# Optimization experiments

Measured on AMD Instinct MI355X. Metric: run time of the kernel, lower is better.

## Reference

```python
import jax, jax.numpy as jnp
import numpy as np

B, C, H, W = 8, 512, 96, 96
CQ = C // 8


def setup_inputs() -> dict:
    key = jax.random.key(0)
    ks = jax.random.split(key, 8)
    s = 1.0 / np.sqrt(C)  # conv-like init scale to keep logits sane
    return {
        "x": jax.random.normal(ks[0], (B, C, H, W), jnp.float32),
        "Wq": jax.random.normal(ks[1], (CQ, C), jnp.float32) * s,
        "bq": jax.random.normal(ks[2], (CQ,), jnp.float32) * s,
        "Wk": jax.random.normal(ks[3], (CQ, C), jnp.float32) * s,
        "bk": jax.random.normal(ks[4], (CQ,), jnp.float32) * s,
        "Wv": jax.random.normal(ks[5], (C, C), jnp.float32) * s,
        "bv": jax.random.normal(ks[6], (C,), jnp.float32) * s,
        "gamma": jax.random.normal(ks[7], (1,), jnp.float32),
    }


def reference(x, Wq, bq, Wk, bk, Wv, bv, gamma):
    # 1x1 convs == per-pixel linear projections
    q = jnp.einsum('bchw,oc->bohw', x, Wq) + bq[None, :, None, None]  # [B,CQ,H,W]
    k = jnp.einsum('bchw,oc->bohw', x, Wk) + bk[None, :, None, None]  # [B,CQ,H,W]
    v = jnp.einsum('bchw,oc->bohw', x, Wv) + bv[None, :, None, None]  # [B,C ,H,W]

    h = x.shape[2]
    # column (vertical) attention logits: query at (h,w) vs keys at (j,w)
    energy_H = jnp.einsum('bchw,bcjw->bhwj', q, k)  # [B,H,W,H]
    # row (horizontal) attention logits: query at (h,w) vs keys at (h,j)
    energy_W = jnp.einsum('bchw,bchj->bhwj', q, k)  # [B,H,W,W]

    att = jax.nn.softmax(jnp.concatenate([energy_H, energy_W], axis=-1), axis=-1)
    att_H = att[..., :h]   # [B,H,W,H]
    att_W = att[..., h:]   # [B,H,W,W]

    out_H = jnp.einsum('bcjw,bhwj->bchw', v, att_H)
    out_W = jnp.einsum('bchj,bhwj->bchw', v, att_W)
    return gamma[0] * (out_H + out_W)
```

## Files before the change

kernel.cpp:

```cpp
#include <hip/hip_runtime.h>

#define B 8
#define C 512
#define H 96
#define W 96
#define HW (H*W)
#define KD 512
#define NSP 9216

typedef __attribute__((ext_vector_type(4))) float f32x4;
typedef __attribute__((ext_vector_type(8))) _Float16 f16x8;

typedef __attribute__((address_space(3))) unsigned int lds_u32;
typedef const __attribute__((address_space(1))) unsigned int glb_u32;
static __device__ __forceinline__ void gload16(const void* gsrc, void* ldst) {
    __builtin_amdgcn_global_load_lds((glb_u32*)gsrc, (lds_u32*)ldst, 16, 0, 0);
}

static __device__ __forceinline__ int tidx(int row, int kgrp) {
    return row * 32 + ((kgrp ^ ((row >> 2) & 3)) << 3);
}
static __device__ __forceinline__ int tidx64(int row, int gr) {
    return row * 64 + ((gr ^ (row & 7)) << 3);
}

__global__ __launch_bounds__(256) void split_w(
    const float* __restrict__ Wv, const float* __restrict__ Wq, const float* __restrict__ Wk,
    _Float16* __restrict__ Wv_h,
    _Float16* __restrict__ Wqk_h, _Float16* __restrict__ Wqk_l)
{
    int i = blockIdx.x * 256 + threadIdx.x;
    if (i < C * C) Wv_h[i] = (_Float16)Wv[i];
    if (i < 128 * C) {
        int m = i / C, k = i % C;
        float f = (m < 64) ? Wq[m * C + k] : Wk[(m - 64) * C + k];
        _Float16 h = (_Float16)f;
        Wqk_h[i] = h;
        Wqk_l[i] = (_Float16)(f - (float)h);
    }
}

__global__ __launch_bounds__(256) void split_x(
    const float* __restrict__ x,
    _Float16* __restrict__ xhT, _Float16* __restrict__ xlT)
{
    __shared__ float t[64][65];
    int n0 = blockIdx.x * 64, k0 = blockIdx.y * 64, b = blockIdx.z;
    int tid = threadIdx.x;
    const float* xb = x + ((size_t)b * KD + k0) * NSP + n0;
    #pragma unroll
    for (int it = 0; it < 4; ++it) {
        int idx = tid + it * 256;
        int kr = idx >> 4, nq = idx & 15;
        float4 v = *(const float4*)&xb[(size_t)kr * NSP + nq * 4];
        t[kr][nq * 4 + 0] = v.x;
        t[kr][nq * 4 + 1] = v.y;
        t[kr][nq * 4 + 2] = v.z;
        t[kr][nq * 4 + 3] = v.w;
    }
    __syncthreads();
    #pragma unroll
    for (int it = 0; it < 2; ++it) {
        int gid = tid + it * 256;
        int n = gid >> 3, g = gid & 7;
        f16x8 hi, lo;
        #pragma unroll
        for (int u = 0; u < 8; ++u) {
            float f = t[g * 8 + u][n];
            _Float16 hh = (_Float16)f;
            hi[u] = hh;
            lo[u] = (_Float16)(f - (float)hh);
        }
        size_t off = ((size_t)b * NSP + n0 + n) * KD + k0 + g * 8;
        *(f16x8*)&xhT[off] = hi;
        *(f16x8*)&xlT[off] = lo;
    }
}

__global__ __launch_bounds__(256, 2) void gemm_v(
    const _Float16* __restrict__ xhT,
    const _Float16* __restrict__ Wh,
    const float* __restrict__ bias,
    _Float16* __restrict__ out16)
{
    __shared__ _Float16 smem[8192];
    const int W_OFF = 0, X_OFF = 4096;

    int tid = threadIdx.x;
    int n0 = blockIdx.x * 128, m0 = blockIdx.y * 128, b = blockIdx.z;
    int lane = tid & 63, wave = tid >> 6;
    int wr = wave >> 1, wc = wave & 1;
    int l15 = lane & 15, l4 = lane >> 4;

    int grow = tid >> 2, gcol = (tid & 3) * 8;
    const _Float16* pW = Wh + (size_t)(m0 + grow) * KD + gcol;
    const _Float16* pX = xhT + ((size_t)b * NSP + n0 + grow) * KD + gcol;
    const size_t half = (size_t)64 * KD;
    int ldsW0 = W_OFF + wave * 512;
    int ldsW1 = W_OFF + 2048 + wave * 512;
    int ldsX0 = X_OFF + wave * 512;
    int ldsX1 = X_OFF + 2048 + wave * 512;

    f32x4 acc[4][4];
    #pragma unroll
    for (int i = 0; i < 4; ++i)
        #pragma unroll
        for (int j = 0; j < 4; ++j)
            acc[i][j] = (f32x4){0.f, 0.f, 0.f, 0.f};

    for (int k0 = 0; k0 < KD; k0 += 32) {
        gload16(pW + k0,        &smem[ldsW0]);
        gload16(pW + half + k0, &smem[ldsW1]);
        gload16(pX + k0,        &smem[ldsX0]);
        gload16(pX + half + k0, &smem[ldsX1]);
        __syncthreads();

        f16x8 af[4], bf[4];
        #pragma unroll
        for (int f = 0; f < 4; ++f) {
            af[f] = *(const f16x8*)&smem[W_OFF + (wr * 64 + f * 16 + l15) * 32 + l4 * 8];
            bf[f] = *(const f16x8*)&smem[X_OFF + (wc * 64 + f * 16 + l15) * 32 + l4 * 8];
        }
        #pragma unroll
        for (int i = 0; i < 4; ++i)
            #pragma unroll
            for (int j = 0; j < 4; ++j)
                acc[i][j] = __builtin_amdgcn_mfma_f32_16x16x32_f16(af[i], bf[j], acc[i][j], 0, 0, 0);
        __syncthreads();
    }

    #pragma unroll
    for (int i = 0; i < 4; ++i)
        #pragma unroll
        for (int r = 0; r < 4; ++r) {
            int row = m0 + wr * 64 + i * 16 + l4 * 4 + r;
            float bv = bias[row];
            #pragma unroll
            for (int j = 0; j < 4; ++j) {
                int col = n0 + wc * 64 + j * 16 + l15;
                out16[((size_t)b * C + row) * NSP + col] = (_Float16)(acc[i][j][r] + bv);
            }
        }
}

__global__ __launch_bounds__(256, 2) void gemm_qk(
    const _Float16* __restrict__ xhT, const _Float16* __restrict__ xlT,
    const _Float16* __restrict__ Wqh, const _Float16* __restrict__ Wql,
    const float* __restrict__ bias0, const float* __restrict__ bias1,
    _Float16* __restrict__ qh, _Float16* __restrict__ ql,
    _Float16* __restrict__ kh, _Float16* __restrict__ kl)
{
    __shared__ _Float16 smem[16384];
    const int XH = 0, XL = 4096, WHo = 8192, WLo = 12288;

    int tid = threadIdx.x;
    int n0 = blockIdx.x * 128, b = blockIdx.z;
    int lane = tid & 63, wave = tid >> 6;
    int wr = wave >> 1, wc = wave & 1;
    int l15 = lane & 15, l4 = lane >> 4;

    int grow = tid >> 2, gcol = (tid & 3) * 8;
    const _Float16* pXh = xhT + ((size_t)b * NSP + n0 + grow) * KD + gcol;
    const _Float16* pXl = xlT + ((size_t)b * NSP + n0 + grow) * KD + gcol;
    const _Float16* pWh = Wqh + (size_t)grow * KD + gcol;
    const _Float16* pWl = Wql + (size_t)grow * KD + gcol;
    const size_t half = (size_t)64 * KD;
    int base0 = wave * 512, base1 = 2048 + wave * 512;

    f32x4 acc[4][4];
    #pragma unroll
    for (int i = 0; i < 4; ++i)
        #pragma unroll
        for (int j = 0; j < 4; ++j)
            acc[i][j] = (f32x4){0.f, 0.f, 0.f, 0.f};

    for (int k0 = 0; k0 < KD; k0 += 32) {
        gload16(pXh + k0,        &smem[XH + base0]);
        gload16(pXh + half + k0, &smem[XH + base1]);
        gload16(pXl + k0,        &smem[XL + base0]);
        gload16(pXl + half + k0, &smem[XL + base1]);
        gload16(pWh + k0,        &smem[WHo + base0]);
        gload16(pWh + half + k0, &smem[WHo + base1]);
        gload16(pWl + k0,        &smem[WLo + base0]);
        gload16(pWl + half + k0, &smem[WLo + base1]);
        __syncthreads();

        f16x8 axh[4], axl[4], bwh[4], bwl[4];
        #pragma unroll
        for (int f = 0; f < 4; ++f) {
            int ra = (wr * 64 + f * 16 + l15) * 32 + l4 * 8;
            int rb = (wc * 64 + f * 16 + l15) * 32 + l4 * 8;
            axh[f] = *(const f16x8*)&smem[XH + ra];
            axl[f] = *(const f16x8*)&smem[XL + ra];
            bwh[f] = *(const f16x8*)&smem[WHo + rb];
            bwl[f] = *(const f16x8*)&smem[WLo + rb];
        }
        #pragma unroll
        for (int i = 0; i < 4; ++i)
            #pragma unroll
            for (int j = 0; j < 4; ++j)
                acc[i][j] = __builtin_amdgcn_mfma_f32_16x16x32_f16(axh[i], bwh[j], acc[i][j], 0, 0, 0);
        #pragma unroll
        for (int i = 0; i < 4; ++i)
            #pragma unroll
            for (int j = 0; j < 4; ++j)
                acc[i][j] = __builtin_amdgcn_mfma_f32_16x16x32_f16(axh[i], bwl[j], acc[i][j], 0, 0, 0);
        #pragma unroll
        for (int i = 0; i < 4; ++i)
            #pragma unroll
            for (int j = 0; j < 4; ++j)
                acc[i][j] = __builtin_amdgcn_mfma_f32_16x16x32_f16(axl[i], bwh[j], acc[i][j], 0, 0, 0);
        __syncthreads();
    }

    #pragma unroll
    for (int i = 0; i < 4; ++i)
        #pragma unroll
        for (int r = 0; r < 4; ++r) {
            int sp = n0 + wr * 64 + i * 16 + l4 * 4 + r;
            #pragma unroll
            for (int j = 0; j < 4; ++j) {
                int wcol = wc * 64 + j * 16 + l15;
                float val = acc[i][j][r] + (wcol < 64 ? bias0[wcol] : bias1[wcol - 64]);
                _Float16 hi = (_Float16)val;
                _Float16 lo = (_Float16)(val - (float)hi);
                size_t off = ((size_t)b * NSP + sp) * 64 + (wcol & 63);
                if (wcol < 64) { qh[off] = hi; ql[off] = lo; }
                else           { kh[off] = hi; kl[off] = lo; }
            }
        }
}

__global__ __launch_bounds__(256, 2) void energy_mfma(
    const _Float16* __restrict__ qh, const _Float16* __restrict__ ql,
    const _Float16* __restrict__ kh, const _Float16* __restrict__ kl,
    float* __restrict__ out, float* __restrict__ part, int pMul, int rMul)
{
    __shared__ _Float16 sm[4 * 96 * 64];
    const int T_QH = 0, T_QL = 6144, T_KH = 12288, T_KL = 18432;
    int p = blockIdx.x, b = blockIdx.y;
    int tid = threadIdx.x;
    size_t base = ((size_t)b * HW + (size_t)p * pMul) * 64;
    size_t rstride = (size_t)rMul * 64;

    #pragma unroll
    for (int tile = 0; tile < 4; ++tile) {
        const _Float16* src = (tile == 0) ? qh : (tile == 1) ? ql : (tile == 2) ? kh : kl;
        int tb = tile * 6144;
        #pragma unroll
        for (int sub = 0; sub < 3; ++sub) {
            int s = sub * 256 + tid;
            int row = s >> 3, g = s & 7;
            f16x8 d = *(const f16x8*)&src[base + row * rstride + g * 8];
            *(f16x8*)&sm[tb + tidx64(row, g)] = d;
        }
    }
    __syncthreads();

    int lane = tid & 63, wave = tid >> 6;
    int wr = wave >> 1, wc = wave & 1;
    int l15 = lane & 15, l4 = lane >> 4;

    f32x4 acc[3][3];
    #pragma unroll
    for (int i = 0; i < 3; ++i)
        #pragma unroll
        for (int j = 0; j < 3; ++j)
            acc[i][j] = (f32x4){0.f, 0.f, 0.f, 0.f};

    #pragma unroll
    for (int ks = 0; ks < 2; ++ks) {
        f16x8 Ah[3], Al[3], Bh[3], Bl[3];
        int gr = ks * 4 + l4;
        #pragma unroll
        for (int i = 0; i < 3; ++i) {
            int sa = tidx64(wr * 48 + i * 16 + l15, gr);
            Ah[i] = *(const f16x8*)&sm[T_QH + sa];
            Al[i] = *(const f16x8*)&sm[T_QL + sa];
            int sb = tidx64(wc * 48 + i * 16 + l15, gr);
            Bh[i] = *(const f16x8*)&sm[T_KH + sb];
            Bl[i] = *(const f16x8*)&sm[T_KL + sb];
        }
        #pragma unroll
        for (int i = 0; i < 3; ++i)
            #pragma unroll
            for (int j = 0; j < 3; ++j) {
                acc[i][j] = __builtin_amdgcn_mfma_f32_16x16x32_f16(Ah[i], Bh[j], acc[i][j], 0, 0, 0);
                acc[i][j] = __builtin_amdgcn_mfma_f32_16x16x32_f16(Ah[i], Bl[j], acc[i][j], 0, 0, 0);
                acc[i][j] = __builtin_amdgcn_mfma_f32_16x16x32_f16(Al[i], Bh[j], acc[i][j], 0, 0, 0);
            }
    }

    size_t ob = (size_t)(b * 96 + p) * 9216;
    #pragma unroll
    for (int i = 0; i < 3; ++i)
        #pragma unroll
        for (int r = 0; r < 4; ++r) {
            int row = wr * 48 + i * 16 + l4 * 4 + r;
            #pragma unroll
            for (int j = 0; j < 3; ++j)
                out[ob + (size_t)row * 96 + wc * 48 + j * 16 + l15] = acc[i][j][r];
        }

    __syncthreads();
    float* scr = (float*)sm;
    #pragma unroll
    for (int i = 0; i < 3; ++i)
        #pragma unroll
        for (int r = 0; r < 4; ++r) {
            int row = wr * 48 + i * 16 + l4 * 4 + r;
            float m3 = fmaxf(fmaxf(acc[i][0][r], acc[i][1][r]), acc[i][2][r]);
            #pragma unroll
            for (int mk = 1; mk < 16; mk <<= 1) m3 = fmaxf(m3, __shfl_xor(m3, mk));
            float s = __expf(acc[i][0][r] - m3) + __expf(acc[i][1][r] - m3) + __expf(acc[i][2][r] - m3);
            #pragma unroll
            for (int mk = 1; mk < 16; mk <<= 1) s += __shfl_xor(s, mk);
            if (l15 == 0) {
                scr[row * 4 + wc * 2]     = m3;
                scr[row * 4 + wc * 2 + 1] = s;
            }
        }
    __syncthreads();
    if (tid < 96) {
        float m0 = scr[tid * 4], s0 = scr[tid * 4 + 1];
        float m1 = scr[tid * 4 + 2], s1 = scr[tid * 4 + 3];
        float M = fmaxf(m0, m1);
        float S = s0 * __expf(m0 - M) + s1 * __expf(m1 - M);
        size_t idx = (pMul == 96) ? ((size_t)b * HW + p * 96 + tid)
                                  : ((size_t)b * HW + tid * 96 + p);
        part[idx * 2]     = M;
        part[idx * 2 + 1] = S;
    }
}

__global__ __launch_bounds__(256) void combine_ms(
    const float* __restrict__ pW, const float* __restrict__ pH,
    const float* __restrict__ gamma, float* __restrict__ ms)
{
    int row = blockIdx.x * 256 + threadIdx.x;
    float mW = pW[row * 2], sW = pW[row * 2 + 1];
    float mH = pH[row * 2], sH = pH[row * 2 + 1];
    float M = fmaxf(mW, mH);
    float S = sW * __expf(mW - M) + sH * __expf(mH - M);
    ms[row * 2]     = M;
    ms[row * 2 + 1] = gamma[0] / S;
}

template<int OUT16>
__global__ __launch_bounds__(256) void agg_mfma(
    const float* __restrict__ E, const float* __restrict__ ms,
    const _Float16* __restrict__ v16,
    float* __restrict__ dstF, _Float16* __restrict__ dstH, int msMode)
{
    __shared__ _Float16 satt[3][96 * 32];

    int r = blockIdx.x, b = blockIdx.y;
    int tid = threadIdx.x;
    int lane = tid & 63, wave = tid >> 6;
    int l15 = lane & 15, l4 = lane >> 4;

    const float* Eb = &E[(size_t)(b * 96 + r) * 9216];
    int msBase = b * HW;
    #pragma unroll
    for (int it = 0; it < 5; ++it) {
        int g_id = tid + it * 256;
        if (g_id < 1152) {
            int s = g_id / 12, gj = g_id % 12;
            int mi = msMode ? (msBase + s * 96 + r) : (msBase + r * 96 + s);
            float m  = ms[(size_t)mi * 2];
            float sc = ms[(size_t)mi * 2 + 1];
            float4 e0 = *(const float4*)&Eb[s * 96 + gj * 8];
            float4 e1 = *(const float4*)&Eb[s * 96 + gj * 8 + 4];
            float pv[8] = {e0.x, e0.y, e0.z, e0.w, e1.x, e1.y, e1.z, e1.w};
            f16x8 ph;
            #pragma unroll
            for (int u = 0; u < 8; ++u)
                ph[u] = (_Float16)(__expf(pv[u] - m) * sc);
            *(f16x8*)&satt[gj >> 2][tidx(s, gj & 3)] = ph;
        }
    }
    __syncthreads();

    const _Float16* vb = v16 + (size_t)b * C * 9216 + r * 96;

    for (int cc = 0; cc < 4; ++cc) {
        int cbase = cc * 128 + wave * 32;
        f32x4 acc[2][6];
        #pragma unroll
        for (int i = 0; i < 2; ++i)
            #pragma unroll
            for (int n = 0; n < 6; ++n)
                acc[i][n] = (f32x4){0.f, 0.f, 0.f, 0.f};

        #pragma unroll
        for (int kc = 0; kc < 3; ++kc) {
            f16x8 af[2];
            #pragma unroll
            for (int i = 0; i < 2; ++i)
                af[i] = *(const f16x8*)&vb[(size_t)(cbase + i * 16 + l15) * 9216 + kc * 32 + l4 * 8];
            f16x8 Bp[6];
            #pragma unroll
            for (int n = 0; n < 6; ++n)
                Bp[n] = *(const f16x8*)&satt[kc][tidx(n * 16 + l15, l4)];
            #pragma unroll
            for (int i = 0; i < 2; ++i)
                #pragma unroll
                for (int n = 0; n < 6; ++n)
                    acc[i][n] = __builtin_amdgcn_mfma_f32_16x16x32_f16(af[i], Bp[n], acc[i][n], 0, 0, 0);
        }

        #pragma unroll
        for (int i = 0; i < 2; ++i)
            #pragma unroll
            for (int r4 = 0; r4 < 4; ++r4) {
                int cl = cbase + i * 16 + l4 * 4 + r4;
                size_t rowb = ((size_t)b * C + cl) * 9216 + r * 96;
                #pragma unroll
                for (int n = 0; n < 6; ++n) {
                    int s = n * 16 + l15;
                    if (OUT16) dstH[rowb + s] = (_Float16)acc[i][n][r4];
                    else       dstF[rowb + s] = acc[i][n][r4];
                }
            }
    }
}

__global__ __launch_bounds__(256) void transpose_f16(
    const _Float16* __restrict__ src, _Float16* __restrict__ dst)
{
    size_t base = (size_t)blockIdx.x * (96 * 96);
    __shared__ _Float16 t[96][97];
    int tid = threadIdx.x;
    for (int i = tid; i < 96 * 96; i += 256) t[i / 96][i % 96] = src[base + i];
    __syncthreads();
    for (int i = tid; i < 96 * 96; i += 256) dst[base + i] = t[i % 96][i / 96];
}

__global__ __launch_bounds__(256) void transpose_add(
    const _Float16* __restrict__ srcT, float* __restrict__ out)
{
    size_t base = (size_t)blockIdx.x * (96 * 96);
    __shared__ _Float16 t[96][97];
    int tid = threadIdx.x;
    for (int i = tid; i < 96 * 96; i += 256) t[i / 96][i % 96] = srcT[base + i];
    __syncthreads();
    for (int i = tid; i < 96 * 96; i += 256) out[base + i] += (float)t[i % 96][i / 96];
}

__global__ __launch_bounds__(256) void combine(
    const _Float16* __restrict__ w16, const _Float16* __restrict__ hT,
    float* __restrict__ out)
{
    size_t base = (size_t)blockIdx.x * (96 * 96);
    __shared__ _Float16 t[96][97];
    int tid = threadIdx.x;
    for (int i = tid; i < 96 * 96; i += 256) t[i / 96][i % 96] = hT[base + i];
    __syncthreads();
    for (int i = tid; i < 96 * 96; i += 256)
        out[base + i] = (float)w16[base + i] + (float)t[i % 96][i / 96];
}

extern "C" void kernel_launch(void* const* d_in, const int* in_sizes, int n_in,
                              void* d_out, int out_size, void* d_ws, size_t ws_size,
                              hipStream_t stream)
{
    const float* x     = (const float*)d_in[0];
    const float* Wq    = (const float*)d_in[1];
    const float* bq    = (const float*)d_in[2];
    const float* Wk    = (const float*)d_in[3];
    const float* bk    = (const float*)d_in[4];
    const float* Wv    = (const float*)d_in[5];
    const float* bv    = (const float*)d_in[6];
    const float* gamma = (const float*)d_in[7];
    float* out = (float*)d_out;

    const size_t NK = (size_t)B * NSP * KD;
    _Float16* xhT = (_Float16*)d_ws;
    _Float16* xlT = xhT + NK;
    _Float16* qh  = xlT + NK;
    _Float16* ql  = qh + (size_t)B * HW * 64;
    _Float16* kh  = ql + (size_t)B * HW * 64;
    _Float16* kl  = kh + (size_t)B * HW * 64;
    float* EHp = (float*)(kl + (size_t)B * HW * 64);
    float* EWp = EHp + (size_t)B * HW * 96;
    float* ms  = (float*)qh;
    _Float16* vA  = xlT;
    _Float16* vB  = xhT;
    _Float16* outHT = xlT;
    float* pW = (float*)xhT;
    float* pH = pW + (size_t)2 * B * HW;

    _Float16* Wv_h  = (_Float16*)EHp;
    _Float16* Wqk_h = Wv_h + (size_t)C * C;
    _Float16* Wqk_l = Wqk_h + (size_t)128 * C;

    const size_t NEED = 245366784ull;
    bool bigws = ws_size >= NEED + NK * sizeof(_Float16);
    _Float16* outW16 = (_Float16*)((char*)d_ws + NEED);

    dim3 blk(256);

    split_w<<<dim3((C*C + 255)/256), blk, 0, stream>>>(Wv, Wq, Wk, Wv_h, Wqk_h, Wqk_l);
    split_x<<<dim3(NSP/64, KD/64, B), blk, 0, stream>>>(x, xhT, xlT);

    gemm_qk<<<dim3(NSP/128, 1, B), blk, 0, stream>>>(xhT, xlT, Wqk_h, Wqk_l, bq, bk, qh, ql, kh, kl);
    gemm_v<<<dim3(NSP/128, C/128, B), blk, 0, stream>>>(xhT, Wv_h, bv, vA);

    energy_mfma<<<dim3(96, B), blk, 0, stream>>>(qh, ql, kh, kl, EWp, pW, 96, 1);
    energy_mfma<<<dim3(96, B), blk, 0, stream>>>(qh, ql, kh, kl, EHp, pH, 1, 96);
    combine_ms<<<dim3(B*HW/256), blk, 0, stream>>>(pW, pH, gamma, ms);

    transpose_f16<<<dim3(B*C), blk, 0, stream>>>(vA, vB);

    if (bigws) {
        agg_mfma<1><<<dim3(96, B), blk, 0, stream>>>(EWp, ms, vA, nullptr, outW16, 0);
        agg_mfma<1><<<dim3(96, B), blk, 0, stream>>>(EHp, ms, vB, nullptr, outHT, 1);
        combine<<<dim3(B*C), blk, 0, stream>>>(outW16, outHT, out);
    } else {
        agg_mfma<0><<<dim3(96, B), blk, 0, stream>>>(EWp, ms, vA, out, nullptr, 0);
        agg_mfma<1><<<dim3(96, B), blk, 0, stream>>>(EHp, ms, vB, nullptr, outHT, 1);
        transpose_add<<<dim3(B*C), blk, 0, stream>>>(outHT, out);
    }
}
```

Before: 378.2 us.

## Store energy logits as max-subtracted fp16, vectorize transposes, add nontemporal memory ops

Energy kernels now subtract the per-row partial max and write the logits as fp16 instead of fp32. This halves the energy write and read traffic, and each agg kernel can exponentiate directly using a per-direction scale precomputed in combine_ms. split_x processes two k-tiles per block with batched loads, and the transpose and combine kernels use 16-byte vector loads and stores. Nontemporal hints are added across many stores. fp16 logits lose some precision, and the row-max exponent trick assumes (logit - partial max) plus a scale stays in range.

```diff
diff --git a/kernel.cpp b/kernel.cpp
--- a/kernel.cpp
+++ b/kernel.cpp
@@ -44,36 +44,43 @@
     const float* __restrict__ x,
     _Float16* __restrict__ xhT, _Float16* __restrict__ xlT)
 {
-    __shared__ float t[64][65];
-    int n0 = blockIdx.x * 64, k0 = blockIdx.y * 64, b = blockIdx.z;
+    __shared__ float t[2][64][65];
+    int n0 = blockIdx.x * 64, k0 = blockIdx.y * 128, b = blockIdx.z;
     int tid = threadIdx.x;
     const float* xb = x + ((size_t)b * KD + k0) * NSP + n0;
+
+    f32x4 v[8];
+    #pragma unroll
+    for (int it = 0; it < 8; ++it) {
+        int idx = tid + it * 256;
+        int tile = idx >> 10, kr = (idx >> 4) & 63, nq = idx & 15;
+        v[it] = __builtin_nontemporal_load(
+            (const f32x4*)&xb[(size_t)(tile * 64 + kr) * NSP + nq * 4]);
+    }
+    #pragma unroll
+    for (int it = 0; it < 8; ++it) {
+        int idx = tid + it * 256;
+        int tile = idx >> 10, kr = (idx >> 4) & 63, nq = idx & 15;
+        #pragma unroll
+        for (int u = 0; u < 4; ++u) t[tile][kr][nq * 4 + u] = v[it][u];
+    }
+    __syncthreads();
     #pragma unroll
     for (int it = 0; it < 4; ++it) {
-        int idx = tid + it * 256;
-        int kr = idx >> 4, nq = idx & 15;
-        float4 v = *(const float4*)&xb[(size_t)kr * NSP + nq * 4];
-        t[kr][nq * 4 + 0] = v.x;
-        t[kr][nq * 4 + 1] = v.y;
-        t[kr][nq * 4 + 2] = v.z;
-        t[kr][nq * 4 + 3] = v.w;
-    }
-    __syncthreads();
-    #pragma unroll
-    for (int it = 0; it < 2; ++it) {
         int gid = tid + it * 256;
-        int n = gid >> 3, g = gid & 7;
+        int tile = gid >> 9, w2 = gid & 511;
+        int n = w2 >> 3, g = w2 & 7;
         f16x8 hi, lo;
         #pragma unroll
         for (int u = 0; u < 8; ++u) {
-            float f = t[g * 8 + u][n];
+            float f = t[tile][g * 8 + u][n];
             _Float16 hh = (_Float16)f;
             hi[u] = hh;
             lo[u] = (_Float16)(f - (float)hh);
         }
-        size_t off = ((size_t)b * NSP + n0 + n) * KD + k0 + g * 8;
-        *(f16x8*)&xhT[off] = hi;
-        *(f16x8*)&xlT[off] = lo;
+        size_t off = ((size_t)b * NSP + n0 + n) * KD + k0 + tile * 64 + g * 8;
+        __builtin_nontemporal_store(hi, (f16x8*)&xhT[off]);
+        __builtin_nontemporal_store(lo, (f16x8*)&xlT[off]);
     }
 }
 
@@ -138,7 +145,8 @@
             #pragma unroll
             for (int j = 0; j < 4; ++j) {
                 int col = n0 + wc * 64 + j * 16 + l15;
-                out16[((size_t)b * C + row) * NSP + col] = (_Float16)(acc[i][j][r] + bv);
+                __builtin_nontemporal_store((_Float16)(acc[i][j][r] + bv),
+                    &out16[((size_t)b * C + row) * NSP + col]);
             }
         }
 }
@@ -234,7 +242,7 @@
 __global__ __launch_bounds__(256, 2) void energy_mfma(
     const _Float16* __restrict__ qh, const _Float16* __restrict__ ql,
     const _Float16* __restrict__ kh, const _Float16* __restrict__ kl,
-    float* __restrict__ out, float* __restrict__ part, int pMul, int rMul)
+    _Float16* __restrict__ out16, float* __restrict__ part, int pMul, int rMul)
 {
     __shared__ _Float16 sm[4 * 96 * 64];
     const int T_QH = 0, T_QL = 6144, T_KH = 12288, T_KL = 18432;
@@ -291,19 +299,9 @@
             }
     }
 
-    size_t ob = (size_t)(b * 96 + p) * 9216;
-    #pragma unroll
-    for (int i = 0; i < 3; ++i)
-        #pragma unroll
-        for (int r = 0; r < 4; ++r) {
-            int row = wr * 48 + i * 16 + l4 * 4 + r;
-            #pragma unroll
-            for (int j = 0; j < 3; ++j)
-                out[ob + (size_t)row * 96 + wc * 48 + j * 16 + l15] = acc[i][j][r];
-        }
-
-    __syncthreads();
-    float* scr = (float*)sm;
+    __syncthreads();
+    float* scr  = (float*)sm;
+    float* scrM = scr + 384;
     #pragma unroll
     for (int i = 0; i < 3; ++i)
         #pragma unroll
@@ -330,25 +328,42 @@
                                   : ((size_t)b * HW + tid * 96 + p);
         part[idx * 2]     = M;
         part[idx * 2 + 1] = S;
-    }
+        scrM[tid] = M;
+    }
+    __syncthreads();
+
+    size_t ob = (size_t)(b * 96 + p) * 9216;
+    #pragma unroll
+    for (int i = 0; i < 3; ++i)
+        #pragma unroll
+        for (int r = 0; r < 4; ++r) {
+            int row = wr * 48 + i * 16 + l4 * 4 + r;
+            float Mrow = scrM[row];
+            #pragma unroll
+            for (int j = 0; j < 3; ++j)
+                __builtin_nontemporal_store((_Float16)(acc[i][j][r] - Mrow),
+                    &out16[ob + (size_t)row * 96 + wc * 48 + j * 16 + l15]);
+        }
 }
 
 __global__ __launch_bounds__(256) void combine_ms(
     const float* __restrict__ pW, const float* __restrict__ pH,
-    const float* __restrict__ gamma, float* __restrict__ ms)
+    const float* __restrict__ gamma,
+    float* __restrict__ msW, float* __restrict__ msH)
 {
     int row = blockIdx.x * 256 + threadIdx.x;
     float mW = pW[row * 2], sW = pW[row * 2 + 1];
     float mH = pH[row * 2], sH = pH[row * 2 + 1];
     float M = fmaxf(mW, mH);
-    float S = sW * __expf(mW - M) + sH * __expf(mH - M);
-    ms[row * 2]     = M;
-    ms[row * 2 + 1] = gamma[0] / S;
+    float eW = __expf(mW - M), eH = __expf(mH - M);
+    float g = gamma[0] / (sW * eW + sH * eH);
+    msW[row] = g * eW;
+    msH[row] = g * eH;
 }
 
 template<int OUT16>
 __global__ __launch_bounds__(256) void agg_mfma(
-    const float* __restrict__ E, const float* __restrict__ ms,
+    const _Float16* __restrict__ E16, const float* __restrict__ msDir,
     const _Float16* __restrict__ v16,
     float* __restrict__ dstF, _Float16* __restrict__ dstH, int msMode)
 {
@@ -359,7 +374,7 @@
     int lane = tid & 63, wave = tid >> 6;
     int l15 = lane & 15, l4 = lane >> 4;
 
-    const float* Eb = &E[(size_t)(b * 96 + r) * 9216];
+    const _Float16* Eb = &E16[(size_t)(b * 96 + r) * 9216];
     int msBase = b * HW;
     #pragma unroll
     for (int it = 0; it < 5; ++it) {
@@ -367,15 +382,12 @@
         if (g_id < 1152) {
             int s = g_id / 12, gj = g_id % 12;
             int mi = msMode ? (msBase + s * 96 + r) : (msBase + r * 96 + s);
-            float m  = ms[(size_t)mi * 2];
-            float sc = ms[(size_t)mi * 2 + 1];
-            float4 e0 = *(const float4*)&Eb[s * 96 + gj * 8];
-            float4 e1 = *(const float4*)&Eb[s * 96 + gj * 8 + 4];
-            float pv[8] = {e0.x, e0.y, e0.z, e0.w, e1.x, e1.y, e1.z, e1.w};
+            float sc = msDir[mi];
+            f16x8 ev = *(const f16x8*)&Eb[s * 96 + gj * 8];
             f16x8 ph;
             #pragma unroll
             for (int u = 0; u < 8; ++u)
-                ph[u] = (_Float16)(__expf(pv[u] - m) * sc);
+                ph[u] = (_Float16)(__expf((float)ev[u]) * sc);
             *(f16x8*)&satt[gj >> 2][tidx(s, gj & 3)] = ph;
         }
     }
@@ -418,8 +430,8 @@
                 #pragma unroll
                 for (int n = 0; n < 6; ++n) {
                     int s = n * 16 + l15;
-                    if (OUT16) dstH[rowb + s] = (_Float16)acc[i][n][r4];
-                    else       dstF[rowb + s] = acc[i][n][r4];
+                    if (OUT16) __builtin_nontemporal_store((_Float16)acc[i][n][r4], &dstH[rowb + s]);
+                    else       __builtin_nontemporal_store(acc[i][n][r4], &dstF[rowb + s]);
                 }
             }
     }
@@ -429,20 +441,34 @@
     const _Float16* __restrict__ src, _Float16* __restrict__ dst)
 {
     size_t base = (size_t)blockIdx.x * (96 * 96);
-    __shared__ _Float16 t[96][97];
-    int tid = threadIdx.x;
-    for (int i = tid; i < 96 * 96; i += 256) t[i / 96][i % 96] = src[base + i];
-    __syncthreads();
-    for (int i = tid; i < 96 * 96; i += 256) dst[base + i] = t[i % 96][i / 96];
+    __shared__ _Float16 t[96][104];
+    int tid = threadIdx.x;
+    for (int g = tid; g < 1152; g += 256) {
+        int row = g / 12, c8 = (g % 12) * 8;
+        f16x8 v = __builtin_nontemporal_load((const f16x8*)&src[base + row * 96 + c8]);
+        *(f16x8*)&t[row][c8] = v;
+    }
+    __syncthreads();
+    for (int g = tid; g < 1152; g += 256) {
+        int row = g / 12, c8 = (g % 12) * 8;
+        f16x8 o;
+        #pragma unroll
+        for (int u = 0; u < 8; ++u) o[u] = t[c8 + u][row];
+        __builtin_nontemporal_store(o, (f16x8*)&dst[base + row * 96 + c8]);
+    }
 }
 
 __global__ __launch_bounds__(256) void transpose_add(
     const _Float16* __restrict__ srcT, float* __restrict__ out)
 {
     size_t base = (size_t)blockIdx.x * (96 * 96);
-    __shared__ _Float16 t[96][97];
-    int tid = threadIdx.x;
-    for (int i = tid; i < 96 * 96; i += 256) t[i / 96][i % 96] = srcT[base + i];
+    __shared__ _Float16 t[96][104];
+    int tid = threadIdx.x;
+    for (int g = tid; g < 1152; g += 256) {
+        int row = g / 12, c8 = (g % 12) * 8;
+        f16x8 v = *(const f16x8*)&srcT[base + row * 96 + c8];
+        *(f16x8*)&t[row][c8] = v;
+    }
     __syncthreads();
     for (int i = tid; i < 96 * 96; i += 256) out[base + i] += (float)t[i % 96][i / 96];
 }
@@ -452,12 +478,25 @@
     float* __restrict__ out)
 {
     size_t base = (size_t)blockIdx.x * (96 * 96);
-    __shared__ _Float16 t[96][97];
-    int tid = threadIdx.x;
-    for (int i = tid; i < 96 * 96; i += 256) t[i / 96][i % 96] = hT[base + i];
-    __syncthreads();
-    for (int i = tid; i < 96 * 96; i += 256)
-        out[base + i] = (float)w16[base + i] + (float)t[i % 96][i / 96];
+    __shared__ _Float16 t[96][104];
+    int tid = threadIdx.x;
+    for (int g = tid; g < 1152; g += 256) {
+        int row = g / 12, c8 = (g % 12) * 8;
+        f16x8 v = __builtin_nontemporal_load((const f16x8*)&hT[base + row * 96 + c8]);
+        *(f16x8*)&t[row][c8] = v;
+    }
+    __syncthreads();
+    for (int g = tid; g < 1152; g += 256) {
+        int row = g / 12, c8 = (g % 12) * 8;
+        f16x8 wv = __builtin_nontemporal_load((const f16x8*)&w16[base + row * 96 + c8]);
+        f32x4 o0, o1;
+        #pragma unroll
+        for (int u = 0; u < 4; ++u) o0[u] = (float)wv[u] + (float)t[c8 + u][row];
+        #pragma unroll
+        for (int u = 0; u < 4; ++u) o1[u] = (float)wv[4 + u] + (float)t[c8 + 4 + u][row];
+        __builtin_nontemporal_store(o0, (f32x4*)&out[base + row * 96 + c8]);
+        __builtin_nontemporal_store(o1, (f32x4*)&out[base + row * 96 + c8 + 4]);
+    }
 }
 
 extern "C" void kernel_launch(void* const* d_in, const int* in_sizes, int n_in,
@@ -481,16 +520,19 @@
     _Float16* ql  = qh + (size_t)B * HW * 64;
     _Float16* kh  = ql + (size_t)B * HW * 64;
     _Float16* kl  = kh + (size_t)B * HW * 64;
-    float* EHp = (float*)(kl + (size_t)B * HW * 64);
-    float* EWp = EHp + (size_t)B * HW * 96;
-    float* ms  = (float*)qh;
+    float* R4f = (float*)(kl + (size_t)B * HW * 64);
+    float* R5f = R4f + (size_t)B * HW * 96;
+    _Float16* EH16 = (_Float16*)R4f;
+    _Float16* EW16 = (_Float16*)R5f;
+    float* msW = (float*)qh;
+    float* msH = msW + (size_t)B * HW;
     _Float16* vA  = xlT;
     _Float16* vB  = xhT;
     _Float16* outHT = xlT;
     float* pW = (float*)xhT;
     float* pH = pW + (size_t)2 * B * HW;
 
-    _Float16* Wv_h  = (_Float16*)EHp;
+    _Float16* Wv_h  = (_Float16*)R4f;
     _Float16* Wqk_h = Wv_h + (size_t)C * C;
     _Float16* Wqk_l = Wqk_h + (size_t)128 * C;
 
@@ -501,24 +543,24 @@
     dim3 blk(256);
 
     split_w<<<dim3((C*C + 255)/256), blk, 0, stream>>>(Wv, Wq, Wk, Wv_h, Wqk_h, Wqk_l);
-    split_x<<<dim3(NSP/64, KD/64, B), blk, 0, stream>>>(x, xhT, xlT);
+    split_x<<<dim3(NSP/64, KD/128, B), blk, 0, stream>>>(x, xhT, xlT);
 
     gemm_qk<<<dim3(NSP/128, 1, B), blk, 0, stream>>>(xhT, xlT, Wqk_h, Wqk_l, bq, bk, qh, ql, kh, kl);
     gemm_v<<<dim3(NSP/128, C/128, B), blk, 0, stream>>>(xhT, Wv_h, bv, vA);
 
-    energy_mfma<<<dim3(96, B), blk, 0, stream>>>(qh, ql, kh, kl, EWp, pW, 96, 1);
-    energy_mfma<<<dim3(96, B), blk, 0, stream>>>(qh, ql, kh, kl, EHp, pH, 1, 96);
-    combine_ms<<<dim3(B*HW/256), blk, 0, stream>>>(pW, pH, gamma, ms);
+    energy_mfma<<<dim3(96, B), blk, 0, stream>>>(qh, ql, kh, kl, EW16, pW, 96, 1);
+    energy_mfma<<<dim3(96, B), blk, 0, stream>>>(qh, ql, kh, kl, EH16, pH, 1, 96);
+    combine_ms<<<dim3(B*HW/256), blk, 0, stream>>>(pW, pH, gamma, msW, msH);
 
     transpose_f16<<<dim3(B*C), blk, 0, stream>>>(vA, vB);
 
     if (bigws) {
-        agg_mfma<1><<<dim3(96, B), blk, 0, stream>>>(EWp, ms, vA, nullptr, outW16, 0);
-        agg_mfma<1><<<dim3(96, B), blk, 0, stream>>>(EHp, ms, vB, nullptr, outHT, 1);
+        agg_mfma<1><<<dim3(96, B), blk, 0, stream>>>(EW16, msW, vA, nullptr, outW16, 0);
+        agg_mfma<1><<<dim3(96, B), blk, 0, stream>>>(EH16, msH, vB, nullptr, outHT, 1);
         combine<<<dim3(B*C), blk, 0, stream>>>(outW16, outHT, out);
     } else {
-        agg_mfma<0><<<dim3(96, B), blk, 0, stream>>>(EWp, ms, vA, out, nullptr, 0);
-        agg_mfma<1><<<dim3(96, B), blk, 0, stream>>>(EHp, ms, vB, nullptr, outHT, 1);
+        agg_mfma<0><<<dim3(96, B), blk, 0, stream>>>(EW16, msW, vA, out, nullptr, 0);
+        agg_mfma<1><<<dim3(96, B), blk, 0, stream>>>(EH16, msH, vB, nullptr, outHT, 1);
         transpose_add<<<dim3(B*C), blk, 0, stream>>>(outHT, out);
     }
 }
```

After: 422.0 us. 11.6% more time.
